# Performance work log

Measured on AMD Instinct MI355X. Metric: run time of the kernel, lower is better.

## Reference

```python
import jax, jax.numpy as jnp
import numpy as np
from jax import lax

DIM = 512
HEADS = 64
EPS_NORM = 1e-12
EPS_BN = 1e-5


def conv1x1(x, w, b):
    # x: [B,Cin,H,W], w: [Cout,Cin,1,1]
    y = lax.conv_general_dilated(x, w, (1, 1), 'SAME',
                                 dimension_numbers=('NCHW', 'OIHW', 'NCHW'))
    return y + b[None, :, None, None]


def dwconv3x3(x, w, b):
    # depthwise: w: [C,1,3,3], groups=C
    c = x.shape[1]
    y = lax.conv_general_dilated(x, w, (1, 1), 'SAME',
                                 dimension_numbers=('NCHW', 'OIHW', 'NCHW'),
                                 feature_group_count=c)
    return y + b[None, :, None, None]


def l2norm(x):
    # normalize along last axis, torch F.normalize semantics
    n = jnp.sqrt(jnp.sum(x * x, axis=-1, keepdims=True))
    return x / jnp.maximum(n, EPS_NORM)


def setup_inputs() -> dict:
    key = jax.random.key(0)
    ks = jax.random.split(key, 12)
    b, c, h, w = 2, DIM, 128, 128
    s = lambda *sh: 0.02
    inp = {
        'hsi': jax.random.normal(ks[0], (b, c, h, w), jnp.float32),
        'lidar': jax.random.normal(ks[1], (b, c, h, w), jnp.float32),
        'hsi_qkv_w': jax.random.normal(ks[2], (3 * c, c, 1, 1), jnp.float32) * 0.02,
        'hsi_qkv_b': jnp.zeros((3 * c,), jnp.float32),
        'lidar_qkv_w': jax.random.normal(ks[3], (3 * c, c, 1, 1), jnp.float32) * 0.02,
        'lidar_qkv_b': jnp.zeros((3 * c,), jnp.float32),
        'hsi_dw_w': jax.random.normal(ks[4], (3 * c, 1, 3, 3), jnp.float32) * 0.1,
        'hsi_dw_b': jnp.zeros((3 * c,), jnp.float32),
        'lidar_dw_w': jax.random.normal(ks[5], (3 * c, 1, 3, 3), jnp.float32) * 0.1,
        'lidar_dw_b': jnp.zeros((3 * c,), jnp.float32),
        'temp1': jnp.ones((HEADS, 1, 1), jnp.float32),
        'temp2': jnp.ones((HEADS, 1, 1), jnp.float32),
        'proj_w': jax.random.normal(ks[6], (c // 8, c // 4, 1, 1), jnp.float32) * 0.1,
        'proj_b': jnp.zeros((c // 8,), jnp.float32),
        'bn_gamma': jnp.ones((c // 8,), jnp.float32),
        'bn_beta': jnp.zeros((c // 8,), jnp.float32),
        'bn_mean': jnp.zeros((c // 8,), jnp.float32),
        'bn_var': jnp.ones((c // 8,), jnp.float32),
    }
    return inp


def reference(hsi, lidar, hsi_qkv_w, hsi_qkv_b, lidar_qkv_w, lidar_qkv_b,
              hsi_dw_w, hsi_dw_b, lidar_dw_w, lidar_dw_b, temp1, temp2,
              proj_w, proj_b, bn_gamma, bn_beta, bn_mean, bn_var):
    b, c, h, w = hsi.shape
    head = HEADS
    ch = c // head  # per-head channel (=8)
    hw = h * w

    def qkv(x, qkv_w, qkv_b, dw_w, dw_b):
        y = conv1x1(x, qkv_w, qkv_b)
        y = dwconv3x3(y, dw_w, dw_b)
        q, k, v = jnp.split(y, 3, axis=1)
        # b (head ch) h w -> b head ch (h w)
        r = lambda t: t.reshape(b, head, ch, hw)
        return r(q), r(k), r(v)

    hq, hk, hv = qkv(hsi, hsi_qkv_w, hsi_qkv_b, hsi_dw_w, hsi_dw_b)
    lq, lk, lv = qkv(lidar, lidar_qkv_w, lidar_qkv_b, lidar_dw_w, lidar_dw_b)

    q1, k2 = l2norm(hq), l2norm(lk)
    q2, k1 = l2norm(lq), l2norm(hk)

    # channel-attention scores: [b, head, ch, ch]
    attn1 = jnp.einsum('bhcn,bhdn->bhcd', q1, k2) * temp1[None]
    attn2 = jnp.einsum('bhcn,bhdn->bhcd', q2, k1) * temp2[None]

    # conv-based score fusion: cat -> 1x1 conv -> BN (eval) -> ReLU
    attn_cat = jnp.concatenate([attn1, attn2], axis=1)  # [b, 2*head, ch, ch]
    fused = conv1x1(attn_cat, proj_w, proj_b)           # [b, head, ch, ch]
    fused = (fused - bn_mean[None, :, None, None]) / jnp.sqrt(bn_var + EPS_BN)[None, :, None, None]
    fused = fused * bn_gamma[None, :, None, None] + bn_beta[None, :, None, None]
    fused = jax.nn.relu(fused)

    a1 = jax.nn.softmax(fused + attn1, axis=-1)
    a2 = jax.nn.softmax(fused + attn2, axis=-1)
    # dropout is identity in eval mode

    hsi_out = jnp.einsum('bhcd,bhdn->bhcn', a1, hv) + hv
    lidar_out = jnp.einsum('bhcd,bhdn->bhcn', a2, lv) + lv

    hsi_out = hsi_out.reshape(b, c, h, w) + hsi
    lidar_out = lidar_out.reshape(b, c, h, w) + lidar
    return hsi_out, lidar_out
```

## Files before the change

kernel.cpp:

```cpp
#include <hip/hip_runtime.h>
#include <hip/hip_bf16.h>

#define B2    2
#define C     512
#define HH    128
#define WW    128
#define HW    16384
#define HEADS 64

typedef __attribute__((ext_vector_type(8))) short bf16x8;
typedef __attribute__((ext_vector_type(4))) float f32x4;
typedef __attribute__((ext_vector_type(4))) unsigned u32x4;

__device__ __forceinline__ float b2f(short s) {
    union { unsigned u; float f; } x;
    x.u = ((unsigned)(unsigned short)s) << 16;
    return x.f;
}
__device__ __forceinline__ short f2b(float f) {
    unsigned u; __builtin_memcpy(&u, &f, 4);
    unsigned r = u + 0x7FFFu + ((u >> 16) & 1u);
    return (short)(r >> 16);
}
__device__ __forceinline__ unsigned cvt_pk(float lo, float hi) {
    unsigned r;
    asm("v_cvt_pk_bf16_f32 %0, %1, %2" : "=v"(r) : "v"(lo), "v"(hi));
    return r;
}

__device__ __forceinline__ void conv8(
    const short* __restrict__ plane, int row, int lane, int cg,
    const float* __restrict__ w9, float bias0, float* o)
{
    #pragma unroll
    for (int i = 0; i < 8; ++i) o[i] = bias0;
    #pragma unroll
    for (int dr = 0; dr < 3; ++dr) {
        const int r2 = row + dr - 1;
        const bool ok = (unsigned)r2 < (unsigned)HH;
        bf16x8 v = {0, 0, 0, 0, 0, 0, 0, 0};
        if (ok) v = *(const bf16x8*)(plane + (size_t)r2 * WW);
        float rv[10];
        #pragma unroll
        for (int j = 0; j < 8; ++j) rv[1 + j] = b2f(v[j]);
        const float lf = __shfl(rv[8], lane - 1);
        const float rt = __shfl(rv[1], lane + 1);
        rv[0] = (cg == 0)  ? 0.f : lf;
        rv[9] = (cg == 15) ? 0.f : rt;
        const float w0 = w9[dr * 3], w1 = w9[dr * 3 + 1], w2 = w9[dr * 3 + 2];
        #pragma unroll
        for (int i = 0; i < 8; ++i)
            o[i] += w0 * rv[i] + w1 * rv[i + 1] + w2 * rv[i + 2];
    }
}

#define BM 128
#define BN 128
#define BK 32
#define LDK 40

struct GemmJob  { const float* X; const float* W; const float* bias; short* Y; int co_off; };
struct GemmJobs { GemmJob j[8]; };

__global__ __launch_bounds__(256) void k_gemm(GemmJobs jobs)
{
    __shared__ __align__(16) short As[BM * LDK];
    __shared__ __align__(16) short Bs[BN * LDK];

    const GemmJob jb = jobs.j[blockIdx.z];
    const float* X    = jb.X;
    const float* Wm   = jb.W;
    const float* bias = jb.bias;
    short*       Y    = jb.Y;
    const int co_off  = jb.co_off;

    const int co0 = blockIdx.x * BM;
    const int p0  = blockIdx.y * BN;

    const int t = threadIdx.x;
    const int lane = t & 63, wv = t >> 6;
    const int wm = (wv & 1) << 6, wn = (wv >> 1) << 6;
    const int l15 = lane & 15, quad = lane >> 4;
    const int rm = t & 127;
    const int kc = (t >> 7) << 4;

    f32x4 acc[4][4] = {};

    for (int kk = 0; kk < C; kk += BK) {
        const float* asrc = Wm + (size_t)(co_off + co0 + rm) * C + kk + kc;
        unsigned au[4];
        #pragma unroll
        for (int j = 0; j < 2; ++j) {
            f32x4 v = *(const f32x4*)(asrc + j * 4);
            au[2 * j]     = cvt_pk(v[0], v[1]);
            au[2 * j + 1] = cvt_pk(v[2], v[3]);
        }
        unsigned au2[4];
        #pragma unroll
        for (int j = 0; j < 2; ++j) {
            f32x4 v = *(const f32x4*)(asrc + 8 + j * 4);
            au2[2 * j]     = cvt_pk(v[0], v[1]);
            au2[2 * j + 1] = cvt_pk(v[2], v[3]);
        }
        const float* bsrc = X + (size_t)(kk + kc) * HW + p0 + rm;
        float bv[16];
        #pragma unroll
        for (int j = 0; j < 16; ++j) bv[j] = bsrc[(size_t)j * HW];
        unsigned bu[8];
        #pragma unroll
        for (int j = 0; j < 8; ++j) bu[j] = cvt_pk(bv[2 * j], bv[2 * j + 1]);

        *(u32x4*)&As[rm * LDK + kc]     = *(const u32x4*)au;
        *(u32x4*)&As[rm * LDK + kc + 8] = *(const u32x4*)au2;
        *(u32x4*)&Bs[rm * LDK + kc]     = *(const u32x4*)bu;
        *(u32x4*)&Bs[rm * LDK + kc + 8] = *(const u32x4*)(bu + 4);
        __syncthreads();

        bf16x8 af[4], bfr[4];
        #pragma unroll
        for (int i = 0; i < 4; ++i)
            af[i]  = *(const bf16x8*)&As[(wm + i * 16 + l15) * LDK + quad * 8];
        #pragma unroll
        for (int i = 0; i < 4; ++i)
            bfr[i] = *(const bf16x8*)&Bs[(wn + i * 16 + l15) * LDK + quad * 8];
        #pragma unroll
        for (int i = 0; i < 4; ++i)
            #pragma unroll
            for (int j = 0; j < 4; ++j)
                acc[i][j] = __builtin_amdgcn_mfma_f32_16x16x32_bf16(af[i], bfr[j], acc[i][j], 0, 0, 0);
        __syncthreads();
    }

    #pragma unroll
    for (int i = 0; i < 4; ++i) {
        #pragma unroll
        for (int r = 0; r < 4; ++r) {
            const int co = co0 + wm + i * 16 + quad * 4 + r;
            const float bv = bias[co_off + co];
            #pragma unroll
            for (int j = 0; j < 4; ++j) {
                const int p = p0 + wn + j * 16 + l15;
                Y[(size_t)co * HW + p] = f2b(acc[i][j][r] + bv);
            }
        }
    }
}

__global__ __launch_bounds__(256) void k_stats(
    const short* __restrict__ qk0,
    const float* __restrict__ dwh_w, const float* __restrict__ dwh_b,
    const float* __restrict__ dwl_w, const float* __restrict__ dwl_b,
    float* __restrict__ dot1, float* __restrict__ dot2, float* __restrict__ sumsq,
    int job0, long long jobstride)
{
    const int chunk = blockIdx.x;
    const int h = blockIdx.y;
    const int job = job0 + blockIdx.z;
    const int b = job >> 1, type = job & 1;
    const short* qk = qk0 + (size_t)jobstride * blockIdx.z;

    const int t = threadIdx.x;
    const int lane = t & 63, w = t >> 6;
    const int ch = lane & 15, g = lane >> 4;
    const bool isq = (ch < 8);

    const float* dw = isq ? (type ? dwl_w : dwh_w) : (type ? dwh_w : dwl_w);
    const float* db = isq ? (type ? dwl_b : dwh_b) : (type ? dwh_b : dwl_b);
    const int crow = isq ? (h * 8 + ch) : (C + h * 8 + ch - 8);
    float w9[9];
    #pragma unroll
    for (int i = 0; i < 9; ++i) w9[i] = dw[crow * 9 + i];
    const float bias0 = db[crow];

    const short* plane = qk + (size_t)(isq ? (h * 8 + ch)
                                           : (C + h * 8 + ch - 8)) * HW;

    f32x4 acc = {0.f, 0.f, 0.f, 0.f};
    float s2 = 0.f;

    for (int cr = 0; cr < 4; ++cr) {
        const int row = chunk * 16 + w * 4 + cr;
        #pragma unroll
        for (int cc = 0; cc < 4; ++cc) {
            const int px0 = cc * 32 + g * 8;
            float o[8];
            #pragma unroll
            for (int i = 0; i < 8; ++i) o[i] = bias0;
            #pragma unroll
            for (int dr = 0; dr < 3; ++dr) {
                const int r2 = row + dr - 1;
                const bool ok = (unsigned)r2 < (unsigned)HH;
                const short* rp = plane + (size_t)r2 * WW;
                bf16x8 v = {0, 0, 0, 0, 0, 0, 0, 0};
                short sl = 0, sr = 0;
                if (ok) {
                    v = *(const bf16x8*)(rp + px0);
                    if (px0 > 0)      sl = rp[px0 - 1];
                    if (px0 + 8 < WW) sr = rp[px0 + 8];
                }
                float rv[10];
                rv[0] = b2f(sl); rv[9] = b2f(sr);
                #pragma unroll
                for (int j = 0; j < 8; ++j) rv[1 + j] = b2f(v[j]);
                const float w0 = w9[dr * 3], w1 = w9[dr * 3 + 1], w2 = w9[dr * 3 + 2];
                #pragma unroll
                for (int i = 0; i < 8; ++i)
                    o[i] += w0 * rv[i] + w1 * rv[i + 1] + w2 * rv[i + 2];
            }
            #pragma unroll
            for (int i = 0; i < 8; ++i) s2 += o[i] * o[i];
            unsigned pu[4];
            #pragma unroll
            for (int p = 0; p < 4; ++p) pu[p] = cvt_pk(o[2 * p], o[2 * p + 1]);
            bf16x8 f; __builtin_memcpy(&f, pu, 16);
            acc = __builtin_amdgcn_mfma_f32_16x16x32_bf16(f, f, acc, 0, 0, 0);
        }
    }

    float* dotp = (type ? dot2 : dot1) + ((size_t)(b * HEADS + h) << 6);
    #pragma unroll
    for (int r = 0; r < 4; ++r) {
        const int rowc = g * 4 + r;
        if (rowc < 8 && ch >= 8)
            atomicAdd(&dotp[rowc * 8 + (ch - 8)], acc[r]);
    }
    s2 += __shfl_down(s2, 32);
    s2 += __shfl_down(s2, 16);
    if (g == 0) {
        float* sp = isq
            ? &sumsq[((type * 2) * 2 + b) * C + h * 8 + ch]
            : &sumsq[((type * 2 + 1) * 2 + b) * C + h * 8 + (ch - 8)];
        atomicAdd(sp, s2);
    }
}

__global__ __launch_bounds__(256) void k_fuse(
    const float* __restrict__ dot1, const float* __restrict__ dot2,
    const float* __restrict__ sumsq,
    const float* __restrict__ temp1, const float* __restrict__ temp2,
    const float* __restrict__ pw, const float* __restrict__ pb,
    const float* __restrict__ g, const float* __restrict__ be,
    const float* __restrict__ mu, const float* __restrict__ var,
    float* __restrict__ a1, float* __restrict__ a2)
{
    __shared__ float cat[128 * 64];
    __shared__ float fus[64 * 64];
    const int b = blockIdx.x;
    const int t = threadIdx.x;
    const float EPS = 1e-12f;

    for (int idx = t; idx < 128 * 64; idx += 256) {
        const int ic = idx >> 6, ij = idx & 63, i = ij >> 3, j = ij & 7;
        const int is2 = ic >> 6, h = ic & 63;
        const float* dp = is2 ? dot2 : dot1;
        const int qkk = is2 * 2, kkk = is2 * 2 + 1;
        const float nq = sqrtf(sumsq[(qkk * 2 + b) * C + h * 8 + i]);
        const float nk = sqrtf(sumsq[(kkk * 2 + b) * C + h * 8 + j]);
        const float tv = is2 ? temp2[h] : temp1[h];
        const float d = dp[((size_t)(b * HEADS + h) << 6) + ij];
        cat[idx] = d / (fmaxf(nq, EPS) * fmaxf(nk, EPS)) * tv;
    }
    __syncthreads();

    for (int idx = t; idx < 64 * 64; idx += 256) {
        const int hd = idx >> 6, ij = idx & 63;
        float acc = pb[hd];
        for (int ic = 0; ic < 128; ++ic)
            acc += pw[hd * 128 + ic] * cat[ic * 64 + ij];
        const float sc = g[hd] / sqrtf(var[hd] + 1e-5f);
        const float v = (acc - mu[hd]) * sc + be[hd];
        fus[idx] = fmaxf(v, 0.f);
    }
    __syncthreads();

    for (int r = t; r < 512; r += 256) {
        const int hd = r >> 3, i = r & 7;
        float v[8], mx, sum;
        mx = -1e30f;
        #pragma unroll
        for (int j = 0; j < 8; ++j) { v[j] = fus[(hd << 6) + i * 8 + j] + cat[(hd << 6) + i * 8 + j]; mx = fmaxf(mx, v[j]); }
        sum = 0.f;
        #pragma unroll
        for (int j = 0; j < 8; ++j) { v[j] = __expf(v[j] - mx); sum += v[j]; }
        #pragma unroll
        for (int j = 0; j < 8; ++j) a1[((size_t)(b * HEADS + hd) << 6) + i * 8 + j] = v[j] / sum;
        mx = -1e30f;
        #pragma unroll
        for (int j = 0; j < 8; ++j) { v[j] = fus[(hd << 6) + i * 8 + j] + cat[((64 + hd) << 6) + i * 8 + j]; mx = fmaxf(mx, v[j]); }
        sum = 0.f;
        #pragma unroll
        for (int j = 0; j < 8; ++j) { v[j] = __expf(v[j] - mx); sum += v[j]; }
        #pragma unroll
        for (int j = 0; j < 8; ++j) a2[((size_t)(b * HEADS + hd) << 6) + i * 8 + j] = v[j] / sum;
    }
}

__global__ __launch_bounds__(256) void k_out(
    const short* __restrict__ v,
    const float* __restrict__ hsi, const float* __restrict__ lidar,
    const float* __restrict__ dwh_w, const float* __restrict__ dwh_b,
    const float* __restrict__ dwl_w, const float* __restrict__ dwl_b,
    const float* __restrict__ a1, const float* __restrict__ a2,
    float* __restrict__ out)
{
    __shared__ float A[64];
    __shared__ float wv[72], bvs[8];
    const int chunk = blockIdx.x, h = blockIdx.y, zb = blockIdx.z;
    const int s = zb >> 1, b = zb & 1;
    const int t = threadIdx.x;

    const float* x   = (s ? lidar : hsi) + (size_t)b * C * HW;
    const float* dww = s ? dwl_w : dwh_w;
    const float* dwb = s ? dwl_b : dwh_b;
    const float* Ag  = (s ? a2 : a1) + ((size_t)(b * HEADS + h) << 6);
    if (t < 64) A[t] = Ag[t] + (((t >> 3) == (t & 7)) ? 1.0f : 0.0f);
    if (t < 72) wv[t] = dww[(2 * C + h * 8) * 9 + t];
    if (t < 8)  bvs[t] = dwb[2 * C + h * 8 + t];
    __syncthreads();

    const int lane = t & 63, cg = t & 15;
    const int row = chunk * 16 + (t >> 4);
    const int col0 = cg << 3;

    const short* ybase = v + ((size_t)(zb * 512 + h * 8)) * HW + col0;
    const float* xbase = x + (size_t)(h * 8) * HW + (size_t)row * WW + col0;
    float* obase = out + ((size_t)((s * B2 + b) * C + h * 8)) * HW + (size_t)row * WW + col0;

    float o[8][8];
    #pragma unroll
    for (int i = 0; i < 8; ++i)
        #pragma unroll
        for (int px = 0; px < 8; ++px) o[i][px] = 0.f;

    #pragma unroll
    for (int d = 0; d < 8; ++d) {
        float vd[8];
        conv8(ybase + (size_t)d * HW, row, lane, cg, wv + d * 9, bvs[d], vd);
        #pragma unroll
        for (int i = 0; i < 8; ++i) {
            const float ad = A[i * 8 + d];
            #pragma unroll
            for (int px = 0; px < 8; ++px) o[i][px] += ad * vd[px];
        }
    }

    #pragma unroll
    for (int i = 0; i < 8; ++i) {
        f32x4 x0 = *(const f32x4*)(xbase + (size_t)i * HW);
        f32x4 x1 = *(const f32x4*)(xbase + (size_t)i * HW + 4);
        f32x4 o0 = { o[i][0] + x0[0], o[i][1] + x0[1], o[i][2] + x0[2], o[i][3] + x0[3] };
        f32x4 o1 = { o[i][4] + x1[0], o[i][5] + x1[1], o[i][6] + x1[2], o[i][7] + x1[3] };
        *(f32x4*)(obase + (size_t)i * HW)     = o0;
        *(f32x4*)(obase + (size_t)i * HW + 4) = o1;
    }
}

extern "C" void kernel_launch(void* const* d_in, const int* in_sizes, int n_in,
                              void* d_out, int out_size, void* d_ws, size_t ws_size,
                              hipStream_t stream)
{
    const float* hsi  = (const float*)d_in[0];
    const float* lidar= (const float*)d_in[1];
    const float* hqw  = (const float*)d_in[2];
    const float* hqb  = (const float*)d_in[3];
    const float* lqw  = (const float*)d_in[4];
    const float* lqb  = (const float*)d_in[5];
    const float* hdw  = (const float*)d_in[6];
    const float* hdb  = (const float*)d_in[7];
    const float* ldw  = (const float*)d_in[8];
    const float* ldb  = (const float*)d_in[9];
    const float* t1   = (const float*)d_in[10];
    const float* t2   = (const float*)d_in[11];
    const float* pw   = (const float*)d_in[12];
    const float* pb   = (const float*)d_in[13];
    const float* bg   = (const float*)d_in[14];
    const float* bb   = (const float*)d_in[15];
    const float* bm   = (const float*)d_in[16];
    const float* bvv  = (const float*)d_in[17];

    char* ws = (char*)d_ws;
    float* dot1  = (float*)ws;
    float* dot2  = dot1 + 2 * HEADS * 64;
    float* sumsq = dot2 + 2 * HEADS * 64;
    float* a1    = sumsq + 4 * 2 * C;
    float* a2    = a1 + 2 * HEADS * 64;
    short* slab  = (short*)(ws + 147456);

    const size_t statbytes = (size_t)(2 * HEADS * 64 * 2 + 4 * 2 * C) * sizeof(float);
    hipMemsetAsync(dot1, 0, statbytes, stream);

    const size_t jobBytes = (size_t)C * HW * sizeof(short);
    const size_t bigNeed  = 147456 + 8 * jobBytes;

    if (ws_size >= bigNeed) {
        GemmJobs jj;
        for (int job = 0; job < 4; ++job) {
            const int b = job >> 1, type = job & 1;
            const float* qx = (type ? lidar : hsi) + (size_t)b * C * HW;
            const float* kx = (type ? hsi : lidar) + (size_t)b * C * HW;
            const float* qw = type ? lqw : hqw;  const float* qb = type ? lqb : hqb;
            const float* kw = type ? hqw : lqw;  const float* kb = type ? hqb : lqb;
            jj.j[2 * job]     = { qx, qw, qb, slab + (size_t)(2 * job) * C * HW,     0 };
            jj.j[2 * job + 1] = { kx, kw, kb, slab + (size_t)(2 * job + 1) * C * HW, C };
        }
        k_gemm<<<dim3(4, 128, 8), 256, 0, stream>>>(jj);
        k_stats<<<dim3(8, 64, 4), 256, 0, stream>>>(
            slab, hdw, hdb, ldw, ldb, dot1, dot2, sumsq,
            0, (long long)(2 * (size_t)C * HW));

        GemmJobs vj;
        vj.j[0] = { hsi,                    hqw, hqb, slab,                      2 * C };
        vj.j[1] = { hsi   + (size_t)C * HW, hqw, hqb, slab + (size_t)C * HW,     2 * C };
        vj.j[2] = { lidar,                  lqw, lqb, slab + (size_t)2 * C * HW, 2 * C };
        vj.j[3] = { lidar + (size_t)C * HW, lqw, lqb, slab + (size_t)3 * C * HW, 2 * C };
        for (int i = 4; i < 8; ++i) vj.j[i] = vj.j[0];
        k_gemm<<<dim3(4, 128, 4), 256, 0, stream>>>(vj);
    } else {
        for (int b = 0; b < 2; ++b) {
            for (int type = 0; type < 2; ++type) {
                const float* qx = (type ? lidar : hsi) + (size_t)b * C * HW;
                const float* kx = (type ? hsi : lidar) + (size_t)b * C * HW;
                const float* qw = type ? lqw : hqw;  const float* qb = type ? lqb : hqb;
                const float* kw = type ? hqw : lqw;  const float* kb = type ? hqb : lqb;
                GemmJobs jj;
                jj.j[0] = { qx, qw, qb, slab,                  0 };
                jj.j[1] = { kx, kw, kb, slab + (size_t)C * HW, C };
                for (int i = 2; i < 8; ++i) jj.j[i] = jj.j[0];
                k_gemm<<<dim3(4, 128, 2), 256, 0, stream>>>(jj);
                k_stats<<<dim3(8, 64, 1), 256, 0, stream>>>(
                    slab, hdw, hdb, ldw, ldb, dot1, dot2, sumsq,
                    b * 2 + type, 0LL);
            }
        }
        GemmJobs vj;
        vj.j[0] = { hsi,                    hqw, hqb, slab,                      2 * C };
        vj.j[1] = { hsi   + (size_t)C * HW, hqw, hqb, slab + (size_t)C * HW,     2 * C };
        vj.j[2] = { lidar,                  lqw, lqb, slab + (size_t)2 * C * HW, 2 * C };
        vj.j[3] = { lidar + (size_t)C * HW, lqw, lqb, slab + (size_t)3 * C * HW, 2 * C };
        for (int i = 4; i < 8; ++i) vj.j[i] = vj.j[0];
        k_gemm<<<dim3(4, 128, 4), 256, 0, stream>>>(vj);
    }

    k_fuse<<<dim3(2, 1, 1), 256, 0, stream>>>(dot1, dot2, sumsq, t1, t2,
                                              pw, pb, bg, bb, bm, bvv, a1, a2);
    k_out<<<dim3(8, 64, 4), 256, 0, stream>>>(slab, hsi, lidar,
                                              hdw, hdb, ldw, ldb, a1, a2,
                                              (float*)d_out);
}
```

Baseline: 853.9 us.

## Merge QKV projections into one GEMM per image and remap workgroups across XCDs

When the workspace is large enough, a new path runs one GEMM per input image that produces all 3C output channels at once. This replaces the separate Q/K GEMM jobs, each of which re-read the input, plus the later V GEMM. k_stats and k_out now take per-job pointers and strides so they can read from the merged slab layout. The GEMM kernel also remaps block IDs so that consecutive logical tiles land on the same XCD, which should improve L2 reuse of the input and weights. The cost is a larger workspace requirement, and the default path changes only if ws_size covers 4×3 planes.

```diff
diff --git a/kernel.cpp b/kernel.cpp
--- a/kernel.cpp
+++ b/kernel.cpp
@@ -67,15 +67,29 @@
     __shared__ __align__(16) short As[BM * LDK];
     __shared__ __align__(16) short Bs[BN * LDK];
 
-    const GemmJob jb = jobs.j[blockIdx.z];
+    unsigned bx = blockIdx.x, by = blockIdx.y, bz = blockIdx.z;
+    {
+        const unsigned nx = gridDim.x, ny = gridDim.y, nz = gridDim.z;
+        const unsigned nwg = nx * ny * nz;
+        if ((nwg & 7u) == 0u) {
+            const unsigned hw = bx + nx * (by + ny * bz);
+            const unsigned lid = (hw & 7u) * (nwg >> 3) + (hw >> 3);
+            bx = lid % nx;
+            const unsigned rest = lid / nx;
+            by = rest % ny;
+            bz = rest / ny;
+        }
+    }
+
+    const GemmJob jb = jobs.j[bz];
     const float* X    = jb.X;
     const float* Wm   = jb.W;
     const float* bias = jb.bias;
     short*       Y    = jb.Y;
     const int co_off  = jb.co_off;
 
-    const int co0 = blockIdx.x * BM;
-    const int p0  = blockIdx.y * BN;
+    const int co0 = bx * BM;
+    const int p0  = by * BN;
 
     const int t = threadIdx.x;
     const int lane = t & 63, wv = t >> 6;
@@ -146,18 +160,20 @@
     }
 }
 
+struct StatsJobs { const short* q[4]; const short* k[4]; };
+
 __global__ __launch_bounds__(256) void k_stats(
-    const short* __restrict__ qk0,
+    StatsJobs sj,
     const float* __restrict__ dwh_w, const float* __restrict__ dwh_b,
     const float* __restrict__ dwl_w, const float* __restrict__ dwl_b,
     float* __restrict__ dot1, float* __restrict__ dot2, float* __restrict__ sumsq,
-    int job0, long long jobstride)
+    int job0)
 {
     const int chunk = blockIdx.x;
     const int h = blockIdx.y;
-    const int job = job0 + blockIdx.z;
+    const int z = blockIdx.z;
+    const int job = job0 + z;
     const int b = job >> 1, type = job & 1;
-    const short* qk = qk0 + (size_t)jobstride * blockIdx.z;
 
     const int t = threadIdx.x;
     const int lane = t & 63, w = t >> 6;
@@ -172,8 +188,8 @@
     for (int i = 0; i < 9; ++i) w9[i] = dw[crow * 9 + i];
     const float bias0 = db[crow];
 
-    const short* plane = qk + (size_t)(isq ? (h * 8 + ch)
-                                           : (C + h * 8 + ch - 8)) * HW;
+    const short* plane = isq ? (sj.q[z] + (size_t)(h * 8 + ch) * HW)
+                             : (sj.k[z] + (size_t)(h * 8 + (ch - 8)) * HW);
 
     f32x4 acc = {0.f, 0.f, 0.f, 0.f};
     float s2 = 0.f;
@@ -296,7 +312,7 @@
 }
 
 __global__ __launch_bounds__(256) void k_out(
-    const short* __restrict__ v,
+    const short* __restrict__ vslab, long long vstride, int vrowoff,
     const float* __restrict__ hsi, const float* __restrict__ lidar,
     const float* __restrict__ dwh_w, const float* __restrict__ dwh_b,
     const float* __restrict__ dwl_w, const float* __restrict__ dwl_b,
@@ -322,7 +338,8 @@
     const int row = chunk * 16 + (t >> 4);
     const int col0 = cg << 3;
 
-    const short* ybase = v + ((size_t)(zb * 512 + h * 8)) * HW + col0;
+    const short* ybase = vslab + (size_t)zb * (size_t)vstride
+                       + (size_t)(vrowoff + h * 8) * HW + col0;
     const float* xbase = x + (size_t)(h * 8) * HW + (size_t)row * WW + col0;
     float* obase = out + ((size_t)((s * B2 + b) * C + h * 8)) * HW + (size_t)row * WW + col0;
 
@@ -389,10 +406,38 @@
     const size_t statbytes = (size_t)(2 * HEADS * 64 * 2 + 4 * 2 * C) * sizeof(float);
     hipMemsetAsync(dot1, 0, statbytes, stream);
 
-    const size_t jobBytes = (size_t)C * HW * sizeof(short);
-    const size_t bigNeed  = 147456 + 8 * jobBytes;
-
-    if (ws_size >= bigNeed) {
+    const size_t planeBytes  = (size_t)C * HW * sizeof(short);
+    const size_t imgBytes    = 3 * planeBytes;
+    const size_t needMerged  = 147456 + 4 * imgBytes;
+    const size_t needR3      = 147456 + 8 * planeBytes;
+
+    const size_t imgS = (size_t)3 * C * HW;
+
+    if (ws_size >= needMerged) {
+        GemmJobs jj;
+        const float* imgs[4] = { hsi, hsi + (size_t)C * HW, lidar, lidar + (size_t)C * HW };
+        const float* wms[4]  = { hqw, hqw, lqw, lqw };
+        const float* bs[4]   = { hqb, hqb, lqb, lqb };
+        for (int img = 0; img < 4; ++img)
+            jj.j[img] = { imgs[img], wms[img], bs[img], slab + (size_t)img * imgS, 0 };
+        for (int i = 4; i < 8; ++i) jj.j[i] = jj.j[0];
+        k_gemm<<<dim3(12, 128, 4), 256, 0, stream>>>(jj);
+
+        StatsJobs sj;
+        for (int job = 0; job < 4; ++job) {
+            const int b = job >> 1, type = job & 1;
+            sj.q[job] = slab + (size_t)(type * 2 + b) * imgS;
+            sj.k[job] = slab + (size_t)((1 - type) * 2 + b) * imgS + (size_t)C * HW;
+        }
+        k_stats<<<dim3(8, 64, 4), 256, 0, stream>>>(
+            sj, hdw, hdb, ldw, ldb, dot1, dot2, sumsq, 0);
+
+        k_fuse<<<dim3(2, 1, 1), 256, 0, stream>>>(dot1, dot2, sumsq, t1, t2,
+                                                  pw, pb, bg, bb, bm, bvv, a1, a2);
+        k_out<<<dim3(8, 64, 4), 256, 0, stream>>>(
+            slab, (long long)imgS, 2 * C, hsi, lidar,
+            hdw, hdb, ldw, ldb, a1, a2, (float*)d_out);
+    } else if (ws_size >= needR3) {
         GemmJobs jj;
         for (int job = 0; job < 4; ++job) {
             const int b = job >> 1, type = job & 1;
@@ -404,9 +449,14 @@
             jj.j[2 * job + 1] = { kx, kw, kb, slab + (size_t)(2 * job + 1) * C * HW, C };
         }
         k_gemm<<<dim3(4, 128, 8), 256, 0, stream>>>(jj);
+
+        StatsJobs sj;
+        for (int job = 0; job < 4; ++job) {
+            sj.q[job] = slab + (size_t)(2 * job) * C * HW;
+            sj.k[job] = slab + (size_t)(2 * job + 1) * C * HW;
+        }
         k_stats<<<dim3(8, 64, 4), 256, 0, stream>>>(
-            slab, hdw, hdb, ldw, ldb, dot1, dot2, sumsq,
-            0, (long long)(2 * (size_t)C * HW));
+            sj, hdw, hdb, ldw, ldb, dot1, dot2, sumsq, 0);
 
         GemmJobs vj;
         vj.j[0] = { hsi,                    hqw, hqb, slab,                      2 * C };
@@ -415,6 +465,12 @@
         vj.j[3] = { lidar + (size_t)C * HW, lqw, lqb, slab + (size_t)3 * C * HW, 2 * C };
         for (int i = 4; i < 8; ++i) vj.j[i] = vj.j[0];
         k_gemm<<<dim3(4, 128, 4), 256, 0, stream>>>(vj);
+
+        k_fuse<<<dim3(2, 1, 1), 256, 0, stream>>>(dot1, dot2, sumsq, t1, t2,
+                                                  pw, pb, bg, bb, bm, bvv, a1, a2);
+        k_out<<<dim3(8, 64, 4), 256, 0, stream>>>(
+            slab, (long long)((size_t)C * HW), 0, hsi, lidar,
+            hdw, hdb, ldw, ldb, a1, a2, (float*)d_out);
     } else {
         for (int b = 0; b < 2; ++b) {
             for (int type = 0; type < 2; ++type) {
@@ -427,9 +483,12 @@
                 jj.j[1] = { kx, kw, kb, slab + (size_t)C * HW, C };
                 for (int i = 2; i < 8; ++i) jj.j[i] = jj.j[0];
                 k_gemm<<<dim3(4, 128, 2), 256, 0, stream>>>(jj);
+                StatsJobs sj;
+                sj.q[0] = slab;
+                sj.k[0] = slab + (size_t)C * HW;
+                for (int i = 1; i < 4; ++i) { sj.q[i] = sj.q[0]; sj.k[i] = sj.k[0]; }
                 k_stats<<<dim3(8, 64, 1), 256, 0, stream>>>(
-                    slab, hdw, hdb, ldw, ldb, dot1, dot2, sumsq,
-                    b * 2 + type, 0LL);
+                    sj, hdw, hdb, ldw, ldb, dot1, dot2, sumsq, b * 2 + type);
             }
         }
         GemmJobs vj;
@@ -439,11 +498,11 @@
         vj.j[3] = { lidar + (size_t)C * HW, lqw, lqb, slab + (size_t)3 * C * HW, 2 * C };
         for (int i = 4; i < 8; ++i) vj.j[i] = vj.j[0];
         k_gemm<<<dim3(4, 128, 4), 256, 0, stream>>>(vj);
-    }
-
-    k_fuse<<<dim3(2, 1, 1), 256, 0, stream>>>(dot1, dot2, sumsq, t1, t2,
-                                              pw, pb, bg, bb, bm, bvv, a1, a2);
-    k_out<<<dim3(8, 64, 4), 256, 0, stream>>>(slab, hsi, lidar,
-                                              hdw, hdb, ldw, ldb, a1, a2,
-                                              (float*)d_out);
-}
+
+        k_fuse<<<dim3(2, 1, 1), 256, 0, stream>>>(dot1, dot2, sumsq, t1, t2,
+                                                  pw, pb, bg, bb, bm, bvv, a1, a2);
+        k_out<<<dim3(8, 64, 4), 256, 0, stream>>>(
+            slab, (long long)((size_t)C * HW), 0, hsi, lidar,
+            hdw, hdb, ldw, ldb, a1, a2, (float*)d_out);
+    }
+}
```

Result: no change. 844.0 us (-1.2%).
